# Optimization experiments

Hardware: AMD Instinct MI355X
Metric: run time of the kernel (lower is better)

## Reference

```python
import jax, jax.numpy as jnp
import numpy as np

S = 32.0
M = 0.35
T = 0.2
EPS = 1e-12  # F.normalize default eps


def _l2_normalize(x, axis):
    n = jnp.sqrt(jnp.sum(x * x, axis=axis, keepdims=True))
    return x / jnp.maximum(n, EPS)


def setup_inputs() -> dict:
    key = jax.random.key(0)
    k1, k2, k3 = jax.random.split(key, 3)
    B, D, C = 512, 512, 100000
    return {
        "input": jax.random.normal(k1, (B, D), dtype=jnp.float32),
        "weight": jax.random.normal(k2, (C, D), dtype=jnp.float32),
        "label": jax.random.randint(k3, (B,), 0, C, dtype=jnp.int64),
    }


def reference(input, weight, label):
    B = input.shape[0]
    # normalized GEMM -> cosine similarities [B, C]
    cos_theta = _l2_normalize(input, 1) @ _l2_normalize(weight, 1).T
    cos_theta = jnp.clip(cos_theta, -1.0, 1.0)
    rows = jnp.arange(B)
    gt = cos_theta[rows, label][:, None]  # [B, 1]
    # MV-AM: boost hard (mis-classified-ish) logits: cos > gt - m
    hard = cos_theta > (gt - M)
    cos_theta = jnp.where(hard, (T + 1.0) * cos_theta + T, cos_theta)
    # easy_margin=False -> final_gt = gt - m; scatter into label column
    final_gt = gt - M
    cos_theta = cos_theta.at[rows, label].set(final_gt[:, 0])
    return cos_theta * S
```

## Files before the change

kernel.cpp:

```cpp
#include <hip/hip_runtime.h>
#include <hip/hip_bf16.h>


#define S_SCALE 32.0f
#define MARGIN  0.35f
#define T_BOOST 0.2f
#define EPSN    1e-12f

constexpr int Bn = 512;
constexpr int Dn = 512;
constexpr int Cn = 100000;
constexpr int BM = 256, BN = 128, BK = 32;
constexpr int PAD = 40;

typedef __attribute__((ext_vector_type(8))) short bf16x8;
typedef __attribute__((ext_vector_type(4))) float f32x4;

static __device__ inline unsigned short f32_bf16(float f) {
    unsigned int u = __float_as_uint(f);
    u += 0x7FFFu + ((u >> 16) & 1u);
    return (unsigned short)(u >> 16);
}

__global__ __launch_bounds__(256) void prep_kernel(const float* __restrict__ in,
                                                   const float* __restrict__ w,
                                                   const int* __restrict__ label,
                                                   float* __restrict__ gt,
                                                   unsigned short* __restrict__ in_p) {
    int b = blockIdx.x, t = threadIdx.x;
    const float* irow = in + (size_t)b * Dn;
    int lab = label[b];
    const float* wrow = w + (size_t)lab * Dn;
    int c = 2 * t;
    float xa = irow[c], xb = irow[c + 1];
    float ya = wrow[c], yb = wrow[c + 1];
    float s_ii = xa*xa + xb*xb, s_ww = ya*ya + yb*yb, s_iw = xa*ya + xb*yb;
    #pragma unroll
    for (int off = 32; off; off >>= 1) {
        s_ii += __shfl_xor(s_ii, off);
        s_ww += __shfl_xor(s_ww, off);
        s_iw += __shfl_xor(s_iw, off);
    }
    __shared__ float r0[4], r1[4], r2[4], bc[1];
    int wid = t >> 6;
    if ((t & 63) == 0) { r0[wid] = s_ii; r1[wid] = s_ww; r2[wid] = s_iw; }
    __syncthreads();
    if (t == 0) {
        float a  = r0[0] + r0[1] + r0[2] + r0[3];
        float cc = r1[0] + r1[1] + r1[2] + r1[3];
        float d  = r2[0] + r2[1] + r2[2] + r2[3];
        float inv_i = 1.0f / fmaxf(sqrtf(a), EPSN);
        float g = d * inv_i / fmaxf(sqrtf(cc), EPSN);
        gt[b] = fminf(fmaxf(g, -1.0f), 1.0f);
        bc[0] = inv_i;
    }
    __syncthreads();
    float inv_i = bc[0];
    int g = b >> 4, l15 = b & 15;
    int s = t >> 4, lk = (t >> 2) & 3, j2 = (t & 3) * 4;
    int lane = lk * 16 + l15;
    unsigned int off = (unsigned)((g << 14) + (s << 10) + (lane << 4)) + j2;
    unsigned int h0 = f32_bf16(xa * inv_i), h1 = f32_bf16(xb * inv_i);
    *(unsigned int*)((char*)in_p + off) = h0 | (h1 << 16);
}

__global__ __launch_bounds__(512) void gemm_kernel(const unsigned short* __restrict__ in_p,
                                                   const float* __restrict__ w,
                                                   const float* __restrict__ gt,
                                                   const int* __restrict__ label,
                                                   float* __restrict__ out) {
    __shared__ unsigned short Bs[2][BN * PAD];
    __shared__ float inv_s[BN];

    int t = threadIdx.x, wid = t >> 6, lane = t & 63;
    int wm = wid >> 1, wn = wid & 1;
    int l15 = lane & 15, lk = lane >> 4;
    int bm = blockIdx.x, bn = blockIdx.y;

    int srow = t >> 2, q = t & 3;
    int rg = bn * BN + srow; if (rg >= Cn) rg = Cn - 1;
    const float* wsrc = w + (size_t)rg * Dn + q * 8;
    char* sdst0 = (char*)&Bs[0][0] + srow * (PAD * 2) + q * 16;
    char* sdst1 = (char*)&Bs[1][0] + srow * (PAD * 2) + q * 16;

    const char* apb = (const char*)in_p + (((bm * 16 + wm * 4)) << 14) + (lane << 4);

    float ss = 0.f;
    f32x4 acc[4][4];
    #pragma unroll
    for (int m = 0; m < 4; ++m)
        #pragma unroll
        for (int n = 0; n < 4; ++n) acc[m][n] = (f32x4){0.f, 0.f, 0.f, 0.f};

    {
        f32x4 b0 = *(const f32x4*)(wsrc);
        f32x4 b1 = *(const f32x4*)(wsrc + 4);
        ss += b0[0]*b0[0] + b0[1]*b0[1] + b0[2]*b0[2] + b0[3]*b0[3]
            + b1[0]*b1[0] + b1[1]*b1[1] + b1[2]*b1[2] + b1[3]*b1[3];
        bf16x8 hv;
        #pragma unroll
        for (int j = 0; j < 4; ++j) { hv[j] = (short)f32_bf16(b0[j]); hv[4+j] = (short)f32_bf16(b1[j]); }
        *(bf16x8*)sdst0 = hv;
    }
    bf16x8 ar[2][4];
    #pragma unroll
    for (int s = 0; s < 2; ++s)
        #pragma unroll
        for (int m = 0; m < 4; ++m)
            ar[s][m] = *(const bf16x8*)(apb + (m << 14) + (s << 10));
    __syncthreads();

    #pragma unroll
    for (int kt = 0; kt < 16; ++kt) {
        f32x4 b0, b1;
        if (kt < 15) {
            b0 = *(const f32x4*)(wsrc + (kt + 1) * BK);
            b1 = *(const f32x4*)(wsrc + (kt + 1) * BK + 4);
        }
        const char* bsb = (const char*)&Bs[kt & 1][0];
        bf16x8 bfrag[4];
        #pragma unroll
        for (int nf = 0; nf < 4; ++nf) {
            int br = wn * 64 + nf * 16 + l15;
            bfrag[nf] = *(const bf16x8*)(bsb + br * (PAD * 2) + lk * 16);
        }
        #pragma unroll
        for (int m = 0; m < 4; ++m)
            #pragma unroll
            for (int nf = 0; nf < 4; ++nf)
                acc[m][nf] = __builtin_amdgcn_mfma_f32_16x16x32_bf16(ar[kt & 1][m], bfrag[nf], acc[m][nf], 0, 0, 0);
        if (kt + 2 < 16) {
            #pragma unroll
            for (int m = 0; m < 4; ++m)
                ar[kt & 1][m] = *(const bf16x8*)(apb + (m << 14) + ((kt + 2) << 10));
        }
        if (kt < 15) {
            ss += b0[0]*b0[0] + b0[1]*b0[1] + b0[2]*b0[2] + b0[3]*b0[3]
                + b1[0]*b1[0] + b1[1]*b1[1] + b1[2]*b1[2] + b1[3]*b1[3];
            bf16x8 hv;
            #pragma unroll
            for (int j = 0; j < 4; ++j) { hv[j] = (short)f32_bf16(b0[j]); hv[4+j] = (short)f32_bf16(b1[j]); }
            *(bf16x8*)(((kt & 1) ? sdst0 : sdst1)) = hv;
        }
        __syncthreads();
    }

    ss += __shfl_xor(ss, 1); ss += __shfl_xor(ss, 2);
    if (q == 0) inv_s[srow] = 1.0f / fmaxf(sqrtf(ss), EPSN);
    __syncthreads();

    float invc[4];
    #pragma unroll
    for (int nf = 0; nf < 4; ++nf) invc[nf] = inv_s[wn * 64 + nf * 16 + l15];

    #pragma unroll
    for (int m = 0; m < 4; ++m) {
        #pragma unroll
        for (int r = 0; r < 4; ++r) {
            int b_row = bm * BM + wm * 64 + m * 16 + lk * 4 + r;
            float thr = gt[b_row] - MARGIN;
            int lab   = label[b_row];
            float gv  = thr * S_SCALE;
            size_t obase = (size_t)b_row * Cn;
            #pragma unroll
            for (int nf = 0; nf < 4; ++nf) {
                int c = bn * BN + wn * 64 + nf * 16 + l15;
                if (c < Cn) {
                    float cosv = acc[m][nf][r] * invc[nf];
                    cosv = fminf(fmaxf(cosv, -1.0f), 1.0f);
                    float o = (cosv > thr) ? ((T_BOOST + 1.0f) * cosv + T_BOOST) : cosv;
                    o *= S_SCALE;
                    if (c == lab) o = gv;
                    out[obase + c] = o;
                }
            }
        }
    }
}

extern "C" void kernel_launch(void* const* d_in, const int* in_sizes, int n_in,
                              void* d_out, int out_size, void* d_ws, size_t ws_size,
                              hipStream_t stream) {
    const float* in  = (const float*)d_in[0];
    const float* w   = (const float*)d_in[1];
    const int* label = (const int*)d_in[2];
    float* out = (float*)d_out;

    char* ws = (char*)d_ws;
    float* gt            = (float*)ws;
    unsigned short* in_p = (unsigned short*)(ws + 4096);

    prep_kernel<<<dim3(Bn), dim3(256), 0, stream>>>(in, w, label, gt, in_p);
    dim3 grid(2, (Cn + BN - 1) / BN);
    gemm_kernel<<<grid, dim3(512), 0, stream>>>(in_p, w, gt, label, out);
}
```

Measured before the change: 191.7 us.

## Pre-pack weights to bf16 MFMA layout and use LDS-free full-batch GEMM

Adds a separate pass that converts the fp32 weight matrix to bf16 in an MFMA-fragment-friendly layout and computes per-class inverse norms. A new GEMM kernel then covers the whole batch of 512 rows per block, loading A and B fragments straight from global memory with register double/quad buffering and no shared memory or barriers. The intent is to read and convert each weight row once instead of once per batch half, and to remove LDS staging and syncs. It costs an extra kernel plus a roughly 100 MB bf16 write and reread, and it needs a large workspace, falling back to the old path when that is not available.

```diff
diff --git a/kernel.cpp b/kernel.cpp
--- a/kernel.cpp
+++ b/kernel.cpp
@@ -10,8 +10,7 @@
 constexpr int Bn = 512;
 constexpr int Dn = 512;
 constexpr int Cn = 100000;
-constexpr int BM = 256, BN = 128, BK = 32;
-constexpr int PAD = 40;
+constexpr int CG = Cn / 16;
 
 typedef __attribute__((ext_vector_type(8))) short bf16x8;
 typedef __attribute__((ext_vector_type(4))) float f32x4;
@@ -64,13 +63,128 @@
     *(unsigned int*)((char*)in_p + off) = h0 | (h1 << 16);
 }
 
-__global__ __launch_bounds__(512) void gemm_kernel(const unsigned short* __restrict__ in_p,
-                                                   const float* __restrict__ w,
-                                                   const float* __restrict__ gt,
-                                                   const int* __restrict__ label,
-                                                   float* __restrict__ out) {
-    __shared__ unsigned short Bs[2][BN * PAD];
-    __shared__ float inv_s[BN];
+__global__ __launch_bounds__(256) void wpack_kernel(const float* __restrict__ w,
+                                                    float* __restrict__ winv,
+                                                    unsigned short* __restrict__ wp) {
+    int wave = blockIdx.x * 4 + (threadIdx.x >> 6);
+    int lane = threadIdx.x & 63;
+    bool valid = wave < CG;
+    int cg = valid ? wave : CG - 1;
+    int c  = cg * 16 + (lane & 15);
+    int lk = lane >> 4;
+    const float* src = w + (size_t)c * Dn + lk * 8;
+    char* dst = (char*)wp + ((size_t)cg << 14) + (lane << 4);
+    float ss = 0.f;
+    #pragma unroll
+    for (int s = 0; s < 16; ++s) {
+        f32x4 v0 = *(const f32x4*)(src + s * 32);
+        f32x4 v1 = *(const f32x4*)(src + s * 32 + 4);
+        ss += v0[0]*v0[0] + v0[1]*v0[1] + v0[2]*v0[2] + v0[3]*v0[3]
+            + v1[0]*v1[0] + v1[1]*v1[1] + v1[2]*v1[2] + v1[3]*v1[3];
+        bf16x8 hv;
+        #pragma unroll
+        for (int j = 0; j < 4; ++j) { hv[j] = (short)f32_bf16(v0[j]); hv[4+j] = (short)f32_bf16(v1[j]); }
+        if (valid) *(bf16x8*)(dst + (s << 10)) = hv;
+    }
+    ss += __shfl_xor(ss, 16); ss += __shfl_xor(ss, 32);
+    if (valid && lk == 0) winv[c] = 1.0f / fmaxf(sqrtf(ss), EPSN);
+}
+
+__global__ __launch_bounds__(512) void gemmB_kernel(const unsigned short* __restrict__ in_p,
+                                                    const unsigned short* __restrict__ wp,
+                                                    const float* __restrict__ winv,
+                                                    const float* __restrict__ gt,
+                                                    const int* __restrict__ label,
+                                                    float* __restrict__ out) {
+    int t = threadIdx.x, wid = t >> 6, lane = t & 63;
+    int wm = wid >> 1, wn = wid & 1;
+    int l15 = lane & 15, lk = lane >> 4;
+    int blk = blockIdx.x;
+
+    const char* ap = (const char*)in_p + ((wm * 8) << 14) + (lane << 4);
+    int cg0 = blk * 4 + wn * 2;
+    int cg0c = cg0 > CG - 2 ? CG - 2 : cg0;
+    const char* bp = (const char*)wp + ((size_t)cg0c << 14) + (lane << 4);
+
+    f32x4 acc[8][2];
+    #pragma unroll
+    for (int m = 0; m < 8; ++m)
+        #pragma unroll
+        for (int n = 0; n < 2; ++n) acc[m][n] = (f32x4){0.f, 0.f, 0.f, 0.f};
+
+    bf16x8 ar[2][8], br[4][2];
+    #pragma unroll
+    for (int s = 0; s < 2; ++s)
+        #pragma unroll
+        for (int m = 0; m < 8; ++m)
+            ar[s][m] = *(const bf16x8*)(ap + (m << 14) + (s << 10));
+    #pragma unroll
+    for (int s = 0; s < 4; ++s)
+        #pragma unroll
+        for (int n = 0; n < 2; ++n)
+            br[s][n] = *(const bf16x8*)(bp + (n << 14) + (s << 10));
+
+    #pragma unroll
+    for (int s = 0; s < 16; ++s) {
+        #pragma unroll
+        for (int m = 0; m < 8; ++m)
+            #pragma unroll
+            for (int n = 0; n < 2; ++n)
+                acc[m][n] = __builtin_amdgcn_mfma_f32_16x16x32_bf16(ar[s & 1][m], br[s & 3][n], acc[m][n], 0, 0, 0);
+        if (s + 2 < 16) {
+            #pragma unroll
+            for (int m = 0; m < 8; ++m)
+                ar[s & 1][m] = *(const bf16x8*)(ap + (m << 14) + ((s + 2) << 10));
+        }
+        if (s + 4 < 16) {
+            #pragma unroll
+            for (int n = 0; n < 2; ++n)
+                br[s & 3][n] = *(const bf16x8*)(bp + (n << 14) + ((s + 4) << 10));
+        }
+    }
+
+    float invc[2];
+    #pragma unroll
+    for (int n = 0; n < 2; ++n) {
+        int c = blk * 64 + wn * 32 + n * 16 + l15;
+        invc[n] = winv[c < Cn ? c : Cn - 1];
+    }
+
+    #pragma unroll
+    for (int m = 0; m < 8; ++m) {
+        #pragma unroll
+        for (int r = 0; r < 4; ++r) {
+            int b_row = wm * 128 + m * 16 + lk * 4 + r;
+            float thr = gt[b_row] - MARGIN;
+            int lab   = label[b_row];
+            float gv  = thr * S_SCALE;
+            size_t obase = (size_t)b_row * Cn;
+            #pragma unroll
+            for (int n = 0; n < 2; ++n) {
+                int c = blk * 64 + wn * 32 + n * 16 + l15;
+                if (c < Cn) {
+                    float cosv = acc[m][n][r] * invc[n];
+                    cosv = fminf(fmaxf(cosv, -1.0f), 1.0f);
+                    float o = (cosv > thr) ? ((T_BOOST + 1.0f) * cosv + T_BOOST) : cosv;
+                    o *= S_SCALE;
+                    if (c == lab) o = gv;
+                    out[obase + c] = o;
+                }
+            }
+        }
+    }
+}
+
+constexpr int BMf = 256, BNf = 128, BKf = 32;
+constexpr int PADf = 40;
+
+__global__ __launch_bounds__(512) void gemm_fb_kernel(const unsigned short* __restrict__ in_p,
+                                                      const float* __restrict__ w,
+                                                      const float* __restrict__ gt,
+                                                      const int* __restrict__ label,
+                                                      float* __restrict__ out) {
+    __shared__ unsigned short Bs[2][BNf * PADf];
+    __shared__ float inv_s[BNf];
 
     int t = threadIdx.x, wid = t >> 6, lane = t & 63;
     int wm = wid >> 1, wn = wid & 1;
@@ -78,10 +192,10 @@
     int bm = blockIdx.x, bn = blockIdx.y;
 
     int srow = t >> 2, q = t & 3;
-    int rg = bn * BN + srow; if (rg >= Cn) rg = Cn - 1;
+    int rg = bn * BNf + srow; if (rg >= Cn) rg = Cn - 1;
     const float* wsrc = w + (size_t)rg * Dn + q * 8;
-    char* sdst0 = (char*)&Bs[0][0] + srow * (PAD * 2) + q * 16;
-    char* sdst1 = (char*)&Bs[1][0] + srow * (PAD * 2) + q * 16;
+    char* sdst0 = (char*)&Bs[0][0] + srow * (PADf * 2) + q * 16;
+    char* sdst1 = (char*)&Bs[1][0] + srow * (PADf * 2) + q * 16;
 
     const char* apb = (const char*)in_p + (((bm * 16 + wm * 4)) << 14) + (lane << 4);
 
@@ -102,37 +216,37 @@
         for (int j = 0; j < 4; ++j) { hv[j] = (short)f32_bf16(b0[j]); hv[4+j] = (short)f32_bf16(b1[j]); }
         *(bf16x8*)sdst0 = hv;
     }
-    bf16x8 ar[2][4];
+    bf16x8 arf[2][4];
     #pragma unroll
     for (int s = 0; s < 2; ++s)
         #pragma unroll
         for (int m = 0; m < 4; ++m)
-            ar[s][m] = *(const bf16x8*)(apb + (m << 14) + (s << 10));
+            arf[s][m] = *(const bf16x8*)(apb + (m << 14) + (s << 10));
     __syncthreads();
 
     #pragma unroll
     for (int kt = 0; kt < 16; ++kt) {
         f32x4 b0, b1;
         if (kt < 15) {
-            b0 = *(const f32x4*)(wsrc + (kt + 1) * BK);
-            b1 = *(const f32x4*)(wsrc + (kt + 1) * BK + 4);
+            b0 = *(const f32x4*)(wsrc + (kt + 1) * BKf);
+            b1 = *(const f32x4*)(wsrc + (kt + 1) * BKf + 4);
         }
         const char* bsb = (const char*)&Bs[kt & 1][0];
         bf16x8 bfrag[4];
         #pragma unroll
         for (int nf = 0; nf < 4; ++nf) {
             int br = wn * 64 + nf * 16 + l15;
-            bfrag[nf] = *(const bf16x8*)(bsb + br * (PAD * 2) + lk * 16);
+            bfrag[nf] = *(const bf16x8*)(bsb + br * (PADf * 2) + lk * 16);
         }
         #pragma unroll
         for (int m = 0; m < 4; ++m)
             #pragma unroll
             for (int nf = 0; nf < 4; ++nf)
-                acc[m][nf] = __builtin_amdgcn_mfma_f32_16x16x32_bf16(ar[kt & 1][m], bfrag[nf], acc[m][nf], 0, 0, 0);
+                acc[m][nf] = __builtin_amdgcn_mfma_f32_16x16x32_bf16(arf[kt & 1][m], bfrag[nf], acc[m][nf], 0, 0, 0);
         if (kt + 2 < 16) {
             #pragma unroll
             for (int m = 0; m < 4; ++m)
-                ar[kt & 1][m] = *(const bf16x8*)(apb + (m << 14) + ((kt + 2) << 10));
+                arf[kt & 1][m] = *(const bf16x8*)(apb + (m << 14) + ((kt + 2) << 10));
         }
         if (kt < 15) {
             ss += b0[0]*b0[0] + b0[1]*b0[1] + b0[2]*b0[2] + b0[3]*b0[3]
@@ -157,14 +271,14 @@
     for (int m = 0; m < 4; ++m) {
         #pragma unroll
         for (int r = 0; r < 4; ++r) {
-            int b_row = bm * BM + wm * 64 + m * 16 + lk * 4 + r;
+            int b_row = bm * BMf + wm * 64 + m * 16 + lk * 4 + r;
             float thr = gt[b_row] - MARGIN;
             int lab   = label[b_row];
             float gv  = thr * S_SCALE;
             size_t obase = (size_t)b_row * Cn;
             #pragma unroll
             for (int nf = 0; nf < 4; ++nf) {
-                int c = bn * BN + wn * 64 + nf * 16 + l15;
+                int c = bn * BNf + wn * 64 + nf * 16 + l15;
                 if (c < Cn) {
                     float cosv = acc[m][nf][r] * invc[nf];
                     cosv = fminf(fmaxf(cosv, -1.0f), 1.0f);
@@ -189,8 +303,18 @@
     char* ws = (char*)d_ws;
     float* gt            = (float*)ws;
     unsigned short* in_p = (unsigned short*)(ws + 4096);
-
-    prep_kernel<<<dim3(Bn), dim3(256), 0, stream>>>(in, w, label, gt, in_p);
-    dim3 grid(2, (Cn + BN - 1) / BN);
-    gemm_kernel<<<grid, dim3(512), 0, stream>>>(in_p, w, gt, label, out);
-}
+    float* winv          = (float*)(ws + 4096 + 524288);
+    unsigned short* wp   = (unsigned short*)(ws + 4096 + 524288 + 400384);
+    const size_t NEED = 4096ull + 524288 + 400384 + (size_t)CG * 16384;
+
+    if (ws_size >= NEED) {
+        wpack_kernel<<<dim3((CG + 3) / 4), dim3(256), 0, stream>>>(w, winv, wp);
+        prep_kernel<<<dim3(Bn), dim3(256), 0, stream>>>(in, w, label, gt, in_p);
+        int nblk = (Cn + 63) / 64;
+        gemmB_kernel<<<dim3(nblk), dim3(512), 0, stream>>>(in_p, wp, winv, gt, label, out);
+    } else {
+        prep_kernel<<<dim3(Bn), dim3(256), 0, stream>>>(in, w, label, gt, in_p);
+        dim3 grid(2, (Cn + BNf - 1) / BNf);
+        gemm_fb_kernel<<<grid, dim3(512), 0, stream>>>(in_p, w, gt, label, out);
+    }
+}
```

Result: slower. 337.2 us (+75.9%).

## Stage A and fp32 W tiles into LDS via direct global-to-LDS loads

Applied to the files above, without the earlier changes.

The GEMM main loop now uses global_load_lds to copy both the packed bf16 input tiles and the raw fp32 weight tiles straight into double-buffered, XOR-swizzled LDS. It replaces the earlier scheme of register-staged weight conversion and register-prefetched A fragments. The fp32-to-bf16 conversion and the weight row sum of squares now happen after the LDS read, per fragment. The aim is to free VGPRs and let the async copies overlap with the MFMAs. In exchange, LDS traffic doubles for fp32 B, both wm warp pairs repeat the conversion of the same B fragments, and LDS use grows to about 64KB per block, which may lower occupancy.

```diff
diff --git a/kernel.cpp b/kernel.cpp
--- a/kernel.cpp
+++ b/kernel.cpp
@@ -10,8 +10,7 @@
 constexpr int Bn = 512;
 constexpr int Dn = 512;
 constexpr int Cn = 100000;
-constexpr int BM = 256, BN = 128, BK = 32;
-constexpr int PAD = 40;
+constexpr int BM = 256, BN = 128;
 
 typedef __attribute__((ext_vector_type(8))) short bf16x8;
 typedef __attribute__((ext_vector_type(4))) float f32x4;
@@ -20,6 +19,12 @@
     unsigned int u = __float_as_uint(f);
     u += 0x7FFFu + ((u >> 16) & 1u);
     return (unsigned short)(u >> 16);
+}
+
+typedef __attribute__((address_space(1))) const unsigned int GUI;
+typedef __attribute__((address_space(3))) unsigned int LUI;
+static __device__ __forceinline__ void gl16(const void* g, void* l) {
+    __builtin_amdgcn_global_load_lds((GUI*)g, (LUI*)l, 16, 0, 0);
 }
 
 __global__ __launch_bounds__(256) void prep_kernel(const float* __restrict__ in,
@@ -69,7 +74,8 @@
                                                    const float* __restrict__ gt,
                                                    const int* __restrict__ label,
                                                    float* __restrict__ out) {
-    __shared__ unsigned short Bs[2][BN * PAD];
+    __shared__ __align__(16) char Ab[2][16384];
+    __shared__ __align__(16) char Bb[2][16384];
     __shared__ float inv_s[BN];
 
     int t = threadIdx.x, wid = t >> 6, lane = t & 63;
@@ -77,76 +83,81 @@
     int l15 = lane & 15, lk = lane >> 4;
     int bm = blockIdx.x, bn = blockIdx.y;
 
-    int srow = t >> 2, q = t & 3;
-    int rg = bn * BN + srow; if (rg >= Cn) rg = Cn - 1;
-    const float* wsrc = w + (size_t)rg * Dn + q * 8;
-    char* sdst0 = (char*)&Bs[0][0] + srow * (PAD * 2) + q * 16;
-    char* sdst1 = (char*)&Bs[1][0] + srow * (PAD * 2) + q * 16;
-
-    const char* apb = (const char*)in_p + (((bm * 16 + wm * 4)) << 14) + (lane << 4);
-
-    float ss = 0.f;
+    const char* asrc = (const char*)in_p + ((size_t)(bm * 16) << 14) + (lane << 4);
+    int g0 = wid * 2, g1 = wid * 2 + 1;
+    int c0 = wid * 2, c1 = wid * 2 + 1;
+    int rmod = lane >> 3;
+    int psrc = (lane & 7) ^ rmod;
+    int r0g = bn * BN + 8 * c0 + rmod; if (r0g >= Cn) r0g = Cn - 1;
+    int r1g = bn * BN + 8 * c1 + rmod; if (r1g >= Cn) r1g = Cn - 1;
+    const char* bsrc0 = (const char*)w + (size_t)r0g * 2048 + psrc * 16;
+    const char* bsrc1 = (const char*)w + (size_t)r1g * 2048 + psrc * 16;
+
+    #define STAGE(kt, buf)                                                        \
+        do {                                                                      \
+            gl16(asrc + ((size_t)g0 << 14) + ((kt) << 10), &Ab[buf][g0*1024 + lane*16]); \
+            gl16(asrc + ((size_t)g1 << 14) + ((kt) << 10), &Ab[buf][g1*1024 + lane*16]); \
+            gl16(bsrc0 + (kt) * 128, &Bb[buf][c0*1024 + lane*16]);                \
+            gl16(bsrc1 + (kt) * 128, &Bb[buf][c1*1024 + lane*16]);                \
+        } while (0)
+
     f32x4 acc[4][4];
     #pragma unroll
     for (int m = 0; m < 4; ++m)
         #pragma unroll
         for (int n = 0; n < 4; ++n) acc[m][n] = (f32x4){0.f, 0.f, 0.f, 0.f};
-
-    {
-        f32x4 b0 = *(const f32x4*)(wsrc);
-        f32x4 b1 = *(const f32x4*)(wsrc + 4);
-        ss += b0[0]*b0[0] + b0[1]*b0[1] + b0[2]*b0[2] + b0[3]*b0[3]
-            + b1[0]*b1[0] + b1[1]*b1[1] + b1[2]*b1[2] + b1[3]*b1[3];
-        bf16x8 hv;
-        #pragma unroll
-        for (int j = 0; j < 4; ++j) { hv[j] = (short)f32_bf16(b0[j]); hv[4+j] = (short)f32_bf16(b1[j]); }
-        *(bf16x8*)sdst0 = hv;
-    }
-    bf16x8 ar[2][4];
-    #pragma unroll
-    for (int s = 0; s < 2; ++s)
-        #pragma unroll
-        for (int m = 0; m < 4; ++m)
-            ar[s][m] = *(const bf16x8*)(apb + (m << 14) + (s << 10));
+    float ssq[4] = {0.f, 0.f, 0.f, 0.f};
+
+    STAGE(0, 0);
     __syncthreads();
 
     #pragma unroll
     for (int kt = 0; kt < 16; ++kt) {
-        f32x4 b0, b1;
-        if (kt < 15) {
-            b0 = *(const f32x4*)(wsrc + (kt + 1) * BK);
-            b1 = *(const f32x4*)(wsrc + (kt + 1) * BK + 4);
+        int cur = kt & 1;
+        if (kt < 15) STAGE(kt + 1, cur ^ 1);
+
+        bf16x8 ar[4];
+        #pragma unroll
+        for (int mf = 0; mf < 4; ++mf)
+            ar[mf] = *(const bf16x8*)&Ab[cur][(wm * 4 + mf) * 1024 + lane * 16];
+
+        bf16x8 bfrag[4];
+        #pragma unroll
+        for (int nf = 0; nf < 4; ++nf) {
+            int r = wn * 64 + nf * 16 + l15;
+            const char* rb = &Bb[cur][r * 128];
+            int q0 = (2 * lk) ^ (r & 7), q1 = (2 * lk + 1) ^ (r & 7);
+            f32x4 v0 = *(const f32x4*)(rb + q0 * 16);
+            f32x4 v1 = *(const f32x4*)(rb + q1 * 16);
+            bf16x8 hv;
+            #pragma unroll
+            for (int j = 0; j < 4; ++j) {
+                hv[j]     = (short)f32_bf16(v0[j]);
+                hv[4 + j] = (short)f32_bf16(v1[j]);
+            }
+            bfrag[nf] = hv;
+            if (wm == 0)
+                ssq[nf] += v0[0]*v0[0] + v0[1]*v0[1] + v0[2]*v0[2] + v0[3]*v0[3]
+                         + v1[0]*v1[0] + v1[1]*v1[1] + v1[2]*v1[2] + v1[3]*v1[3];
         }
-        const char* bsb = (const char*)&Bs[kt & 1][0];
-        bf16x8 bfrag[4];
-        #pragma unroll
-        for (int nf = 0; nf < 4; ++nf) {
-            int br = wn * 64 + nf * 16 + l15;
-            bfrag[nf] = *(const bf16x8*)(bsb + br * (PAD * 2) + lk * 16);
-        }
-        #pragma unroll
-        for (int m = 0; m < 4; ++m)
+
+        #pragma unroll
+        for (int mf = 0; mf < 4; ++mf)
             #pragma unroll
             for (int nf = 0; nf < 4; ++nf)
-                acc[m][nf] = __builtin_amdgcn_mfma_f32_16x16x32_bf16(ar[kt & 1][m], bfrag[nf], acc[m][nf], 0, 0, 0);
-        if (kt + 2 < 16) {
-            #pragma unroll
-            for (int m = 0; m < 4; ++m)
-                ar[kt & 1][m] = *(const bf16x8*)(apb + (m << 14) + ((kt + 2) << 10));
+                acc[mf][nf] = __builtin_amdgcn_mfma_f32_16x16x32_bf16(ar[mf], bfrag[nf], acc[mf][nf], 0, 0, 0);
+
+        __syncthreads();
+    }
+
+    if (wm == 0) {
+        #pragma unroll
+        for (int nf = 0; nf < 4; ++nf) {
+            float s = ssq[nf];
+            s += __shfl_xor(s, 16); s += __shfl_xor(s, 32);
+            if (lk == 0) inv_s[wn * 64 + nf * 16 + l15] = 1.0f / fmaxf(sqrtf(s), EPSN);
         }
-        if (kt < 15) {
-            ss += b0[0]*b0[0] + b0[1]*b0[1] + b0[2]*b0[2] + b0[3]*b0[3]
-                + b1[0]*b1[0] + b1[1]*b1[1] + b1[2]*b1[2] + b1[3]*b1[3];
-            bf16x8 hv;
-            #pragma unroll
-            for (int j = 0; j < 4; ++j) { hv[j] = (short)f32_bf16(b0[j]); hv[4+j] = (short)f32_bf16(b1[j]); }
-            *(bf16x8*)(((kt & 1) ? sdst0 : sdst1)) = hv;
-        }
-        __syncthreads();
-    }
-
-    ss += __shfl_xor(ss, 1); ss += __shfl_xor(ss, 2);
-    if (q == 0) inv_s[srow] = 1.0f / fmaxf(sqrtf(ss), EPSN);
+    }
     __syncthreads();
 
     float invc[4];
@@ -154,10 +165,10 @@
     for (int nf = 0; nf < 4; ++nf) invc[nf] = inv_s[wn * 64 + nf * 16 + l15];
 
     #pragma unroll
-    for (int m = 0; m < 4; ++m) {
+    for (int mf = 0; mf < 4; ++mf) {
         #pragma unroll
         for (int r = 0; r < 4; ++r) {
-            int b_row = bm * BM + wm * 64 + m * 16 + lk * 4 + r;
+            int b_row = bm * BM + wm * 64 + mf * 16 + lk * 4 + r;
             float thr = gt[b_row] - MARGIN;
             int lab   = label[b_row];
             float gv  = thr * S_SCALE;
@@ -166,7 +177,7 @@
             for (int nf = 0; nf < 4; ++nf) {
                 int c = bn * BN + wn * 64 + nf * 16 + l15;
                 if (c < Cn) {
-                    float cosv = acc[m][nf][r] * invc[nf];
+                    float cosv = acc[mf][nf][r] * invc[nf];
                     cosv = fminf(fmaxf(cosv, -1.0f), 1.0f);
                     float o = (cosv > thr) ? ((T_BOOST + 1.0f) * cosv + T_BOOST) : cosv;
                     o *= S_SCALE;
```

Measured after the change: 239.2 us. 1.25x slower.
